# Optimization experiments

Measured on AMD Instinct MI355X. Metric: run time of the kernel, lower is better.

## Reference

```python
import jax, jax.numpy as jnp
import numpy as np

B, S, E, H = 1, 8192, 1024, 16
D = E // H
SEG_LENS = [2048, 4096, 8192]
DILATIONS = [1, 2, 4]


def setup_inputs() -> dict:
    key = jax.random.key(0)
    k0, k1, k2 = jax.random.split(key, 3)
    sc_in = 1.0 / np.sqrt(E)
    return {
        "x": jax.random.normal(k0, (B, S, E), jnp.float32),
        "w_qkv": jax.random.normal(k1, (3 * E, E), jnp.float32) * sc_in,
        "b_qkv": jnp.zeros((3 * E,), jnp.float32),
        "w_out": jax.random.normal(k2, (E, E), jnp.float32) * sc_in,
        "b_out": jnp.zeros((E,), jnp.float32),
    }


def _sdpa(q, k, v):
    # q,k,v: [B,H,N,D]; standard scaled dot-product attention (non-causal)
    scale = 1.0 / np.sqrt(q.shape[-1])
    scores = jnp.einsum('bhqd,bhkd->bhqk', q, k) * scale
    probs = jax.nn.softmax(scores, axis=-1)
    return jnp.einsum('bhqk,bhkd->bhqd', probs, v)


def reference(x, w_qkv, b_qkv, w_out, b_out):
    # QKV projection: torch Linear is x @ W^T + b
    qkv = x @ w_qkv.T + b_qkv                       # [B,S,3E]
    qkv = qkv.reshape(B, S, 3, H, D).transpose(2, 0, 3, 1, 4)  # [3,B,H,S,D]
    q, k, v = qkv[0], qkv[1], qkv[2]

    seg_outputs = []
    for seg_len, dil in zip(SEG_LENS, DILATIONS):
        if seg_len > S:
            continue
        if dil > 1:
            n = min(seg_len, S // dil)
            pos = np.arange(0, n * dil, dil)        # strided dilated gather
        else:
            pos = np.arange(seg_len)                # leading segment
        o = _sdpa(q[:, :, pos], k[:, :, pos], v[:, :, pos])
        # scatter back to full length (zero elsewhere); also handles zero-padding
        full = jnp.zeros((B, H, S, D), x.dtype).at[:, :, pos, :].set(o)
        seg_outputs.append(full)

    if len(seg_outputs) == 0:
        out = jnp.zeros((B, H, S, D), x.dtype)
    else:
        out = seg_outputs[0]
        for so in seg_outputs[1:]:
            out = out + so
        out = out / len(seg_outputs)                # stack(...).mean(0)

    out = out.transpose(0, 2, 1, 3).reshape(B, S, E)
    return out @ w_out.T + b_out
```

## Files before the change

### kernel.cpp

```cpp
#include <hip/hip_runtime.h>


typedef __attribute__((ext_vector_type(8))) short bf16x8;
typedef __attribute__((ext_vector_type(4))) float f32x4;

#define MFMA(a, b, c) __builtin_amdgcn_mfma_f32_16x16x32_bf16((a), (b), (c), 0, 0, 0)

#if __has_builtin(__builtin_amdgcn_exp2f)
#define EXP2(x) __builtin_amdgcn_exp2f(x)
#else
#define EXP2(x) exp2f(x)
#endif

static __device__ __forceinline__ unsigned short f2bf(float f) {
  unsigned int u = __float_as_uint(f);
  unsigned int r = (u + 0x7FFFu + ((u >> 16) & 1u)) >> 16;
  return (unsigned short)r;
}

__global__ void cvt_f32_bf16(const float* __restrict__ in,
                             unsigned short* __restrict__ out, int n8) {
  int i = blockIdx.x * blockDim.x + threadIdx.x;
  if (i >= n8) return;
  const float4* p = (const float4*)in + (size_t)i * 2;
  float4 a = p[0];
  float4 b = p[1];
  union { bf16x8 v; unsigned short u[8]; } o;
  o.u[0] = f2bf(a.x); o.u[1] = f2bf(a.y); o.u[2] = f2bf(a.z); o.u[3] = f2bf(a.w);
  o.u[4] = f2bf(b.x); o.u[5] = f2bf(b.y); o.u[6] = f2bf(b.z); o.u[7] = f2bf(b.w);
  *((bf16x8*)out + i) = o.v;
}

template <int EPILOGUE>
__global__ __launch_bounds__(256, 2) void gemm_bt(
    const unsigned short* __restrict__ A, const unsigned short* __restrict__ B,
    const float* __restrict__ bias, void* __restrict__ Cout, int N, int K) {
  __shared__ unsigned short At[128 * 32];
  __shared__ unsigned short Bt[128 * 32];
  const int tid = threadIdx.x;
  const int wave = tid >> 6, lane = tid & 63;
  const int quad = lane >> 4, lc = lane & 15;
  const int wm = (wave >> 1) * 64, wn = (wave & 1) * 64;
  const int m0 = blockIdx.x * 128, n0 = blockIdx.y * 128;

  f32x4 acc[4][4] = {};

  for (int k0 = 0; k0 < K; k0 += 32) {
    __syncthreads();
#pragma unroll
    for (int issue = 0; issue < 2; ++issue) {
      const int cbase = issue * 256 + wave * 64;
      const int c = cbase + lane;
      const int row = c >> 2, col8 = (c & 3) * 8;
      __builtin_amdgcn_global_load_lds(
          (const __attribute__((address_space(1))) void*)&A[(size_t)(m0 + row) * K + k0 + col8],
          (__attribute__((address_space(3))) void*)&At[cbase * 8], 16, 0, 0);
      __builtin_amdgcn_global_load_lds(
          (const __attribute__((address_space(1))) void*)&B[(size_t)(n0 + row) * K + k0 + col8],
          (__attribute__((address_space(3))) void*)&Bt[cbase * 8], 16, 0, 0);
    }
    __syncthreads();
    bf16x8 af[4], bfr[4];
#pragma unroll
    for (int t = 0; t < 4; ++t)
      af[t] = *(const bf16x8*)&At[(wm + t * 16 + lc) * 32 + quad * 8];
#pragma unroll
    for (int t = 0; t < 4; ++t)
      bfr[t] = *(const bf16x8*)&Bt[(wn + t * 16 + lc) * 32 + quad * 8];
#pragma unroll
    for (int i = 0; i < 4; ++i)
#pragma unroll
      for (int j = 0; j < 4; ++j)
        acc[i][j] = MFMA(af[i], bfr[j], acc[i][j]);
  }

#pragma unroll
  for (int i = 0; i < 4; ++i) {
#pragma unroll
    for (int j = 0; j < 4; ++j) {
      const int gcol = n0 + wn + j * 16 + lc;
      const float bs = bias[gcol];
#pragma unroll
      for (int r = 0; r < 4; ++r) {
        const int grow = m0 + wm + i * 16 + quad * 4 + r;
        const float v = acc[i][j][r] + bs;
        if (EPILOGUE == 0) {
          const int which = gcol >> 10, rem = gcol & 1023;
          const int hh = rem >> 6, d = rem & 63;
          const float vs = (which == 0) ? v * 0.18033688f : v;
          ((unsigned short*)Cout)[(((size_t)(which * 16 + hh)) * 8192 + grow) * 64 + d] = f2bf(vs);
        } else {
          ((float*)Cout)[(size_t)grow * N + gcol] = v;
        }
      }
    }
  }
}

__global__ void transpose_v(const unsigned short* __restrict__ v,
                            unsigned short* __restrict__ vt1,
                            unsigned short* __restrict__ vt2,
                            unsigned short* __restrict__ vt3) {
  __shared__ unsigned short Tt[64 * 72];
  const int tid = threadIdx.x;
  const int h = blockIdx.y;
  const int bx = blockIdx.x;
  const unsigned short* src = v + (size_t)h * 8192 * 64;
  unsigned short* dst;
  int dil, Nk, t0;
  if (bx < 32)      { dst = vt1; dil = 1; Nk = 2048; t0 = bx; }
  else if (bx < 96) { dst = vt2; dil = 2; Nk = 4096; t0 = bx - 32; }
  else              { dst = vt3; dil = 4; Nk = 2048; t0 = bx - 96; }
  dst += (size_t)h * 64 * Nk;
  const int j0 = t0 * 64;
#pragma unroll
  for (int it = 0; it < 2; ++it) {
    const int slot = tid + it * 256;
    const int jj = slot >> 3, c8 = (slot & 7) * 8;
    *(bf16x8*)&Tt[jj * 72 + c8] =
        *(const bf16x8*)&src[(size_t)(j0 + jj) * dil * 64 + c8];
  }
  __syncthreads();
  const int d = tid >> 2, pg = (tid & 3) * 16;
  union { bf16x8 v2[2]; unsigned short u[16]; } ob;
#pragma unroll
  for (int t = 0; t < 16; ++t) {
    const int pos = pg + t;
    const int w = pos & 31;
    const int jj = (pos & 32) | (((w >> 2) & 1) * 16 + (w >> 3) * 4 + (w & 3));
    ob.u[t] = Tt[jj * 72 + d];
  }
  *(bf16x8*)&dst[(size_t)d * Nk + j0 + pg] = ob.v2[0];
  *(bf16x8*)&dst[(size_t)d * Nk + j0 + pg + 8] = ob.v2[1];
}

__global__ __launch_bounds__(256, 2) void flash_all(
    const unsigned short* __restrict__ qkvb,
    const unsigned short* __restrict__ vt1, float* __restrict__ o1,
    const unsigned short* __restrict__ vt2, float* __restrict__ o2,
    const unsigned short* __restrict__ vt3, float* __restrict__ o3) {
  __shared__ unsigned short Smem[2 * 64 * 64];
  unsigned short* Kt = Smem;
  unsigned short* Vt = Smem + 64 * 64;

  const int bx = blockIdx.x;
  int z, h, qt;
  if ((bx & 1) == 0) { const int i = bx >> 1; z = 1; h = i >> 4; qt = i & 15; }
  else { const int j = bx >> 1; z = (j & 1) ? 2 : 0; const int i = j >> 1; h = i >> 3; qt = i & 7; }
  const int Nk = (z == 1) ? 4096 : 2048;
  const int dil = 1 << z;
  const unsigned short* vt = (z == 0) ? vt1 : (z == 1) ? vt2 : vt3;
  float* o = (z == 0) ? o1 : (z == 1) ? o2 : o3;

  const int tid = threadIdx.x;
  const int wave = tid >> 6, lane = tid & 63;
  const int quad = lane >> 4, lc = lane & 15;

  const unsigned short* qh = qkvb + (size_t)h * 8192 * 64;
  const unsigned short* kh = qkvb + (size_t)(16 + h) * 8192 * 64;
  const unsigned short* vh = vt + (size_t)h * 64 * Nk;

  bf16x8 qf[4][2];
#pragma unroll
  for (int mb = 0; mb < 4; ++mb) {
    const size_t qrow = (size_t)(qt * 256 + wave * 64 + mb * 16 + lc) * dil;
    qf[mb][0] = *(const bf16x8*)&qh[qrow * 64 + quad * 8];
    qf[mb][1] = *(const bf16x8*)&qh[qrow * 64 + quad * 8 + 32];
  }

  union { bf16x8 v; unsigned short u[8]; } one_u;
#pragma unroll
  for (int t = 0; t < 8; ++t) one_u.u[t] = 0x3F80;
  const bf16x8 vone = one_u.v;

  f32x4 oacc[4][4] = {};
  f32x4 lacc[4] = {};

  const int srow = tid >> 3, scol = tid & 7;
  const int swz = (scol ^ (srow & 7)) * 8;

  bf16x8 kg0 = *(const bf16x8*)&kh[(size_t)(srow * dil) * 64 + scol * 8];
  bf16x8 kg1 = *(const bf16x8*)&kh[(size_t)((srow + 32) * dil) * 64 + scol * 8];
  bf16x8 vg0 = *(const bf16x8*)&vh[(size_t)srow * Nk + scol * 8];
  bf16x8 vg1 = *(const bf16x8*)&vh[(size_t)(srow + 32) * Nk + scol * 8];

  for (int kb = 0; kb < Nk; kb += 64) {
    __syncthreads();
    *(bf16x8*)&Kt[srow * 64 + swz] = kg0;
    *(bf16x8*)&Kt[(srow + 32) * 64 + swz] = kg1;
    *(bf16x8*)&Vt[srow * 64 + swz] = vg0;
    *(bf16x8*)&Vt[(srow + 32) * 64 + swz] = vg1;
    __syncthreads();

    if (kb + 64 < Nk) {
      const int nk = kb + 64;
      kg0 = *(const bf16x8*)&kh[(size_t)((nk + srow) * dil) * 64 + scol * 8];
      kg1 = *(const bf16x8*)&kh[(size_t)((nk + srow + 32) * dil) * 64 + scol * 8];
      vg0 = *(const bf16x8*)&vh[(size_t)srow * Nk + nk + scol * 8];
      vg1 = *(const bf16x8*)&vh[(size_t)(srow + 32) * Nk + nk + scol * 8];
    }

#pragma unroll
    for (int ks = 0; ks < 2; ++ks) {
      f32x4 st[2][4];
#pragma unroll
      for (int t = 0; t < 2; ++t) {
        const int row = (ks * 2 + t) * 16 + lc;
        const bf16x8 ka0 = *(const bf16x8*)&Kt[row * 64 + ((quad ^ (lc & 7)) * 8)];
        const bf16x8 ka1 = *(const bf16x8*)&Kt[row * 64 + (((4 + quad) ^ (lc & 7)) * 8)];
#pragma unroll
        for (int mb = 0; mb < 4; ++mb) {
          f32x4 zz = {};
          zz = MFMA(ka0, qf[mb][0], zz);
          st[t][mb] = MFMA(ka1, qf[mb][1], zz);
        }
      }

      bf16x8 pb[4];
#pragma unroll
      for (int mb = 0; mb < 4; ++mb) {
        union { bf16x8 v; unsigned int u[4]; } pu;
#pragma unroll
        for (int t = 0; t < 2; ++t) {
          const unsigned int a0 = __float_as_uint(EXP2(st[t][mb][0])) + 0x8000u;
          const unsigned int a1 = __float_as_uint(EXP2(st[t][mb][1])) + 0x8000u;
          const unsigned int a2 = __float_as_uint(EXP2(st[t][mb][2])) + 0x8000u;
          const unsigned int a3 = __float_as_uint(EXP2(st[t][mb][3])) + 0x8000u;
          pu.u[t * 2 + 0] = __builtin_amdgcn_perm(a1, a0, 0x07060302u);
          pu.u[t * 2 + 1] = __builtin_amdgcn_perm(a3, a2, 0x07060302u);
        }
        pb[mb] = pu.v;
      }

#pragma unroll
      for (int nb = 0; nb < 4; ++nb) {
        const int vrow = nb * 16 + lc;
        const bf16x8 va = *(const bf16x8*)&Vt[vrow * 64 + (((ks * 4 + quad) ^ (lc & 7)) * 8)];
#pragma unroll
        for (int mb = 0; mb < 4; ++mb)
          oacc[mb][nb] = MFMA(va, pb[mb], oacc[mb][nb]);
      }
#pragma unroll
      for (int mb = 0; mb < 4; ++mb) lacc[mb] = MFMA(vone, pb[mb], lacc[mb]);
    }
  }

  __syncthreads();
  float* W = (float*)Smem + wave * 16 * 64;
  const int g = lane >> 2, s4 = lane & 3;
#pragma unroll
  for (int mb = 0; mb < 4; ++mb) {
    const float inv = 1.0f / (3.0f * lacc[mb][0]);
#pragma unroll
    for (int nb = 0; nb < 4; ++nb) {
      const int c = nb * 4 + quad;
      const int cs = (c & 8) | ((c & 7) ^ (lc & 7));
      f32x4 val = oacc[mb][nb];
      val *= inv;
      *(f32x4*)&W[lc * 64 + cs * 4] = val;
    }
    const size_t base = (size_t)(qt * 256 + wave * 64 + mb * 16 + g) * 1024 +
                        (size_t)((bx & 1) ? ((bx >> 1) >> 1) >> 3 : (bx >> 1) >> 4) * 64 + s4 * 16;
#pragma unroll
    for (int c2 = 0; c2 < 4; ++c2) {
      const int c = s4 * 4 + c2;
      const int cs = (c & 8) | ((c & 7) ^ (g & 7));
      *(float4*)&o[base + c2 * 4] = *(const float4*)&W[g * 64 + cs * 4];
    }
  }
}

__global__ void combine(const float* __restrict__ o1, const float* __restrict__ o2,
                        const float* __restrict__ o3,
                        unsigned short* __restrict__ a3b) {
  const int idx = blockIdx.x * 256 + threadIdx.x;
  const int s = idx >> 7, e = (idx & 127) * 8;
  float acc[8] = {};
  if (s < 2048) {
    const float* p = &o1[(size_t)s * 1024 + e];
#pragma unroll
    for (int t = 0; t < 8; ++t) acc[t] += p[t];
  }
  if (!(s & 1)) {
    const float* p = &o2[(size_t)(s >> 1) * 1024 + e];
#pragma unroll
    for (int t = 0; t < 8; ++t) acc[t] += p[t];
  }
  if (!(s & 3)) {
    const float* p = &o3[(size_t)(s >> 2) * 1024 + e];
#pragma unroll
    for (int t = 0; t < 8; ++t) acc[t] += p[t];
  }
  union { bf16x8 v; unsigned short u[8]; } ob;
#pragma unroll
  for (int t = 0; t < 8; ++t) ob.u[t] = f2bf(acc[t]);
  *(bf16x8*)&a3b[(size_t)s * 1024 + e] = ob.v;
}

extern "C" void kernel_launch(void* const* d_in, const int* in_sizes, int n_in,
                              void* d_out, int out_size, void* d_ws, size_t ws_size,
                              hipStream_t stream) {
  const float* x     = (const float*)d_in[0];
  const float* w_qkv = (const float*)d_in[1];
  const float* b_qkv = (const float*)d_in[2];
  const float* w_out = (const float*)d_in[3];
  const float* b_out = (const float*)d_in[4];
  float* out = (float*)d_out;

  char* ws = (char*)d_ws;
  unsigned short* qkvb  = (unsigned short*)(ws);
  float*          o1    = (float*)(ws + 33554432);
  float*          o3    = (float*)(ws + 41943040);
  unsigned short* vt1   = (unsigned short*)(ws + 50331648);
  unsigned short* vt2   = (unsigned short*)(ws + 54525952);
  unsigned short* vt3   = (unsigned short*)(ws + 62914560);
  float*          o2    = (float*)(ws + 67108864);
  unsigned short* wqkvb = (unsigned short*)(ws + 83886080);
  unsigned short* woutb = (unsigned short*)(ws + 90177536);
  unsigned short* xb    = (unsigned short*)(ws + 92274688);
  unsigned short* a3b   = xb;

  cvt_f32_bf16<<<dim3(8388608 / 8 / 256), dim3(256), 0, stream>>>(x, xb, 8388608 / 8);
  cvt_f32_bf16<<<dim3(3145728 / 8 / 256), dim3(256), 0, stream>>>(w_qkv, wqkvb, 3145728 / 8);
  cvt_f32_bf16<<<dim3(1048576 / 8 / 256), dim3(256), 0, stream>>>(w_out, woutb, 1048576 / 8);

  gemm_bt<0><<<dim3(64, 24), dim3(256), 0, stream>>>(xb, wqkvb, b_qkv, qkvb, 3072, 1024);

  transpose_v<<<dim3(128, 16), dim3(256), 0, stream>>>(qkvb + (size_t)32 * 8192 * 64,
                                                       vt1, vt2, vt3);

  flash_all<<<dim3(512), dim3(256), 0, stream>>>(qkvb, vt1, o1, vt2, o2, vt3, o3);

  combine<<<dim3(4096), dim3(256), 0, stream>>>(o1, o2, o3, a3b);

  gemm_bt<1><<<dim3(64, 8), dim3(256), 0, stream>>>(a3b, woutb, b_out, out, 1024, 1024);
}
```

Baseline: 335.0 us.

## Split flash attention key dimension across two wave groups per block

```diff
diff --git a/kernel.cpp b/kernel.cpp
--- a/kernel.cpp
+++ b/kernel.cpp
@@ -134,12 +134,12 @@
   *(bf16x8*)&dst[(size_t)d * Nk + j0 + pg + 8] = ob.v2[1];
 }
 
-__global__ __launch_bounds__(256, 2) void flash_all(
+__global__ __launch_bounds__(512, 4) void flash_all(
     const unsigned short* __restrict__ qkvb,
     const unsigned short* __restrict__ vt1, float* __restrict__ o1,
     const unsigned short* __restrict__ vt2, float* __restrict__ o2,
     const unsigned short* __restrict__ vt3, float* __restrict__ o3) {
-  __shared__ unsigned short Smem[2 * 64 * 64];
+  __shared__ unsigned short Smem[2 * 64 * 64 * 2 + 128];
   unsigned short* Kt = Smem;
   unsigned short* Vt = Smem + 64 * 64;
 
@@ -155,6 +155,7 @@
   const int tid = threadIdx.x;
   const int wave = tid >> 6, lane = tid & 63;
   const int quad = lane >> 4, lc = lane & 15;
+  const int ks = wave >> 2, wq = wave & 3;
 
   const unsigned short* qh = qkvb + (size_t)h * 8192 * 64;
   const unsigned short* kh = qkvb + (size_t)(16 + h) * 8192 * 64;
@@ -163,7 +164,7 @@
   bf16x8 qf[4][2];
 #pragma unroll
   for (int mb = 0; mb < 4; ++mb) {
-    const size_t qrow = (size_t)(qt * 256 + wave * 64 + mb * 16 + lc) * dil;
+    const size_t qrow = (size_t)(qt * 256 + wq * 64 + mb * 16 + lc) * dil;
     qf[mb][0] = *(const bf16x8*)&qh[qrow * 64 + quad * 8];
     qf[mb][1] = *(const bf16x8*)&qh[qrow * 64 + quad * 8 + 32];
   }
@@ -179,94 +180,100 @@
   const int srow = tid >> 3, scol = tid & 7;
   const int swz = (scol ^ (srow & 7)) * 8;
 
-  bf16x8 kg0 = *(const bf16x8*)&kh[(size_t)(srow * dil) * 64 + scol * 8];
-  bf16x8 kg1 = *(const bf16x8*)&kh[(size_t)((srow + 32) * dil) * 64 + scol * 8];
-  bf16x8 vg0 = *(const bf16x8*)&vh[(size_t)srow * Nk + scol * 8];
-  bf16x8 vg1 = *(const bf16x8*)&vh[(size_t)(srow + 32) * Nk + scol * 8];
+  bf16x8 kg = *(const bf16x8*)&kh[(size_t)(srow * dil) * 64 + scol * 8];
+  bf16x8 vg = *(const bf16x8*)&vh[(size_t)srow * Nk + scol * 8];
 
   for (int kb = 0; kb < Nk; kb += 64) {
     __syncthreads();
-    *(bf16x8*)&Kt[srow * 64 + swz] = kg0;
-    *(bf16x8*)&Kt[(srow + 32) * 64 + swz] = kg1;
-    *(bf16x8*)&Vt[srow * 64 + swz] = vg0;
-    *(bf16x8*)&Vt[(srow + 32) * 64 + swz] = vg1;
+    *(bf16x8*)&Kt[srow * 64 + swz] = kg;
+    *(bf16x8*)&Vt[srow * 64 + swz] = vg;
     __syncthreads();
 
     if (kb + 64 < Nk) {
       const int nk = kb + 64;
-      kg0 = *(const bf16x8*)&kh[(size_t)((nk + srow) * dil) * 64 + scol * 8];
-      kg1 = *(const bf16x8*)&kh[(size_t)((nk + srow + 32) * dil) * 64 + scol * 8];
-      vg0 = *(const bf16x8*)&vh[(size_t)srow * Nk + nk + scol * 8];
-      vg1 = *(const bf16x8*)&vh[(size_t)(srow + 32) * Nk + nk + scol * 8];
-    }
-
-#pragma unroll
-    for (int ks = 0; ks < 2; ++ks) {
-      f32x4 st[2][4];
+      kg = *(const bf16x8*)&kh[(size_t)((nk + srow) * dil) * 64 + scol * 8];
+      vg = *(const bf16x8*)&vh[(size_t)srow * Nk + nk + scol * 8];
+    }
+
+    f32x4 st[2][4];
+#pragma unroll
+    for (int t = 0; t < 2; ++t) {
+      const int row = (ks * 2 + t) * 16 + lc;
+      const bf16x8 ka0 = *(const bf16x8*)&Kt[row * 64 + ((quad ^ (lc & 7)) * 8)];
+      const bf16x8 ka1 = *(const bf16x8*)&Kt[row * 64 + (((4 + quad) ^ (lc & 7)) * 8)];
+#pragma unroll
+      for (int mb = 0; mb < 4; ++mb) {
+        f32x4 zz = {};
+        zz = MFMA(ka0, qf[mb][0], zz);
+        st[t][mb] = MFMA(ka1, qf[mb][1], zz);
+      }
+    }
+
+    bf16x8 pb[4];
+#pragma unroll
+    for (int mb = 0; mb < 4; ++mb) {
+      union { bf16x8 v; unsigned int u[4]; } pu;
 #pragma unroll
       for (int t = 0; t < 2; ++t) {
-        const int row = (ks * 2 + t) * 16 + lc;
-        const bf16x8 ka0 = *(const bf16x8*)&Kt[row * 64 + ((quad ^ (lc & 7)) * 8)];
-        const bf16x8 ka1 = *(const bf16x8*)&Kt[row * 64 + (((4 + quad) ^ (lc & 7)) * 8)];
-#pragma unroll
-        for (int mb = 0; mb < 4; ++mb) {
-          f32x4 zz = {};
-          zz = MFMA(ka0, qf[mb][0], zz);
-          st[t][mb] = MFMA(ka1, qf[mb][1], zz);
-        }
-      }
-
-      bf16x8 pb[4];
-#pragma unroll
-      for (int mb = 0; mb < 4; ++mb) {
-        union { bf16x8 v; unsigned int u[4]; } pu;
-#pragma unroll
-        for (int t = 0; t < 2; ++t) {
-          const unsigned int a0 = __float_as_uint(EXP2(st[t][mb][0])) + 0x8000u;
-          const unsigned int a1 = __float_as_uint(EXP2(st[t][mb][1])) + 0x8000u;
-          const unsigned int a2 = __float_as_uint(EXP2(st[t][mb][2])) + 0x8000u;
-          const unsigned int a3 = __float_as_uint(EXP2(st[t][mb][3])) + 0x8000u;
-          pu.u[t * 2 + 0] = __builtin_amdgcn_perm(a1, a0, 0x07060302u);
-          pu.u[t * 2 + 1] = __builtin_amdgcn_perm(a3, a2, 0x07060302u);
-        }
-        pb[mb] = pu.v;
-      }
-
+        const unsigned int a0 = __float_as_uint(EXP2(st[t][mb][0])) + 0x8000u;
+        const unsigned int a1 = __float_as_uint(EXP2(st[t][mb][1])) + 0x8000u;
+        const unsigned int a2 = __float_as_uint(EXP2(st[t][mb][2])) + 0x8000u;
+        const unsigned int a3 = __float_as_uint(EXP2(st[t][mb][3])) + 0x8000u;
+        pu.u[t * 2 + 0] = __builtin_amdgcn_perm(a1, a0, 0x07060302u);
+        pu.u[t * 2 + 1] = __builtin_amdgcn_perm(a3, a2, 0x07060302u);
+      }
+      pb[mb] = pu.v;
+    }
+
+#pragma unroll
+    for (int nb = 0; nb < 4; ++nb) {
+      const int vrow = nb * 16 + lc;
+      const bf16x8 va = *(const bf16x8*)&Vt[vrow * 64 + (((ks * 4 + quad) ^ (lc & 7)) * 8)];
+#pragma unroll
+      for (int mb = 0; mb < 4; ++mb)
+        oacc[mb][nb] = MFMA(va, pb[mb], oacc[mb][nb]);
+    }
+#pragma unroll
+    for (int mb = 0; mb < 4; ++mb) lacc[mb] = MFMA(vone, pb[mb], lacc[mb]);
+  }
+
+  __syncthreads();
+  float* Wo = (float*)Smem + wq * 16 * 64;
+  float* Wp = (float*)Smem + 4096 + wq * 16 * 64;
+  float* lbuf = (float*)Smem + 8192;
+  const int g = lane >> 2, s4 = lane & 3;
+#pragma unroll
+  for (int mb = 0; mb < 4; ++mb) {
+    if (wave >= 4) {
 #pragma unroll
       for (int nb = 0; nb < 4; ++nb) {
-        const int vrow = nb * 16 + lc;
-        const bf16x8 va = *(const bf16x8*)&Vt[vrow * 64 + (((ks * 4 + quad) ^ (lc & 7)) * 8)];
-#pragma unroll
-        for (int mb = 0; mb < 4; ++mb)
-          oacc[mb][nb] = MFMA(va, pb[mb], oacc[mb][nb]);
-      }
-#pragma unroll
-      for (int mb = 0; mb < 4; ++mb) lacc[mb] = MFMA(vone, pb[mb], lacc[mb]);
-    }
-  }
-
-  __syncthreads();
-  float* W = (float*)Smem + wave * 16 * 64;
-  const int g = lane >> 2, s4 = lane & 3;
-#pragma unroll
-  for (int mb = 0; mb < 4; ++mb) {
-    const float inv = 1.0f / (3.0f * lacc[mb][0]);
-#pragma unroll
-    for (int nb = 0; nb < 4; ++nb) {
-      const int c = nb * 4 + quad;
-      const int cs = (c & 8) | ((c & 7) ^ (lc & 7));
-      f32x4 val = oacc[mb][nb];
-      val *= inv;
-      *(f32x4*)&W[lc * 64 + cs * 4] = val;
-    }
-    const size_t base = (size_t)(qt * 256 + wave * 64 + mb * 16 + g) * 1024 +
-                        (size_t)((bx & 1) ? ((bx >> 1) >> 1) >> 3 : (bx >> 1) >> 4) * 64 + s4 * 16;
-#pragma unroll
-    for (int c2 = 0; c2 < 4; ++c2) {
-      const int c = s4 * 4 + c2;
-      const int cs = (c & 8) | ((c & 7) ^ (g & 7));
-      *(float4*)&o[base + c2 * 4] = *(const float4*)&W[g * 64 + cs * 4];
-    }
+        const int c = nb * 4 + quad;
+        const int cs = (c & 8) | ((c & 7) ^ (lc & 7));
+        *(f32x4*)&Wp[lc * 64 + cs * 4] = oacc[mb][nb];
+      }
+      if (quad == 0) lbuf[wq * 16 + lc] = lacc[mb][0];
+    }
+    __syncthreads();
+    if (wave < 4) {
+      const float inv = 1.0f / (3.0f * (lacc[mb][0] + lbuf[wq * 16 + lc]));
+#pragma unroll
+      for (int nb = 0; nb < 4; ++nb) {
+        const int c = nb * 4 + quad;
+        const int cs = (c & 8) | ((c & 7) ^ (lc & 7));
+        f32x4 val = oacc[mb][nb] + *(const f32x4*)&Wp[lc * 64 + cs * 4];
+        val *= inv;
+        *(f32x4*)&Wo[lc * 64 + cs * 4] = val;
+      }
+      const size_t base = (size_t)(qt * 256 + wq * 64 + mb * 16 + g) * 1024 +
+                          (size_t)h * 64 + s4 * 16;
+#pragma unroll
+      for (int c2 = 0; c2 < 4; ++c2) {
+        const int c = s4 * 4 + c2;
+        const int cs = (c & 8) | ((c & 7) ^ (g & 7));
+        *(float4*)&o[base + c2 * 4] = *(const float4*)&Wo[g * 64 + cs * 4];
+      }
+    }
+    __syncthreads();
   }
 }
 
@@ -329,7 +336,7 @@
   transpose_v<<<dim3(128, 16), dim3(256), 0, stream>>>(qkvb + (size_t)32 * 8192 * 64,
                                                        vt1, vt2, vt3);
 
-  flash_all<<<dim3(512), dim3(256), 0, stream>>>(qkvb, vt1, o1, vt2, o2, vt3, o3);
+  flash_all<<<dim3(512), dim3(512), 0, stream>>>(qkvb, vt1, o1, vt2, o2, vt3, o3);
 
   combine<<<dim3(4096), dim3(256), 0, stream>>>(o1, o2, o3, a3b);
 
```

Result: slower. 1.052 ms (+213.9%).
